# Performance work log

Hardware: AMD Instinct MI355X
Metric: run time of the kernel (lower is better)

Reference implementation:

```python
import jax, jax.numpy as jnp
import numpy as np

B = 1024
N_NODES = 30
E_PER = 82
IN_F = 128
HID = 256
HEADS = (3, 2, 1)
N_EH = 41


def _lin(k, fi, fo):
    s = 1.0 / np.sqrt(fi)
    kw, kb = jax.random.split(k)
    W = jax.random.uniform(kw, (fi, fo), jnp.float32, -s, s)
    b = jax.random.uniform(kb, (fo,), jnp.float32, -s, s)
    return W, b


def setup_inputs() -> dict:
    key = jax.random.key(0)
    ks = list(jax.random.split(key, 32))
    rng = np.random.default_rng(0)
    # base 30-node graph with E_PER directed edges, no self-loops
    src = rng.integers(0, N_NODES, E_PER)
    dst = (src + rng.integers(1, N_NODES, E_PER)) % N_NODES
    base = np.stack([src, dst])  # [2, E_PER]
    offs = (np.arange(B) * N_NODES)[None, None, :]  # [1,1,B]
    ei = (base[:, :, None] + offs).transpose(0, 2, 1).reshape(2, -1)  # [2, B*E_PER]
    e_h = rng.choice(E_PER, N_EH, replace=False)
    d = {}
    d["x"] = jax.random.normal(ks[0], (B * N_NODES, IN_F), jnp.float32)
    d["edge_index"] = jnp.asarray(ei, dtype=jnp.int32)
    d["e_h_pairs"] = jnp.asarray(base[:, e_h].T, dtype=jnp.int32)  # [N_EH, 2]
    d["Wp"], d["bp"] = _lin(ks[1], IN_F, HID)
    i = 2
    for l, H in enumerate(HEADS):
        d[f"ln_g{l}"] = jnp.ones((HID,), jnp.float32)
        d[f"ln_b{l}"] = jnp.zeros((HID,), jnp.float32)
        d[f"Wl{l}"], d[f"bl{l}"] = _lin(ks[i], HID, H * HID); i += 1
        d[f"Wr{l}"], d[f"br{l}"] = _lin(ks[i], HID, H * HID); i += 1
        d[f"att{l}"] = jax.random.normal(ks[i], (H, HID), jnp.float32) * 0.1; i += 1
        d[f"bias{l}"] = jnp.zeros((HID,), jnp.float32)
    dims = [2 * HID, 256, 128, 128, 1]
    for j in range(4):
        d[f"Wm{j}"], d[f"bm{j}"] = _lin(ks[i], dims[j], dims[j + 1]); i += 1
    return d


def _layer_norm(h, g, b):
    mu = jnp.mean(h, -1, keepdims=True)
    var = jnp.mean((h - mu) ** 2, -1, keepdims=True)
    return (h - mu) * jax.lax.rsqrt(var + 1e-5) * g + b


def _gatv2(h, src, dst, n, Wl, bl, Wr, br, att, bias):
    # PyG GATv2Conv, concat=False (mean over heads), self-loops already in src/dst
    H, C = att.shape
    xl = (h @ Wl + bl).reshape(-1, H, C)  # source transform
    xr = (h @ Wr + br).reshape(-1, H, C)  # target transform
    xj = xl[src]                          # [E,H,C]
    e = jax.nn.leaky_relu(xj + xr[dst], 0.2)
    logits = jnp.einsum('ehc,hc->eh', e, att)  # [E,H]
    m = jax.lax.stop_gradient(jax.ops.segment_max(logits, dst, num_segments=n))
    ex = jnp.exp(logits - m[dst])
    denom = jax.ops.segment_sum(ex, dst, num_segments=n)
    alpha = ex / denom[dst]               # softmax over incoming edges of dst
    out = jax.ops.segment_sum(xj * alpha[..., None], dst, num_segments=n)  # [N,H,C]
    return jnp.mean(out, 1) + bias


def reference(x, edge_index, e_h_pairs, Wp, bp,
              ln_g0, ln_b0, Wl0, bl0, Wr0, br0, att0, bias0,
              ln_g1, ln_b1, Wl1, bl1, Wr1, br1, att1, bias1,
              ln_g2, ln_b2, Wl2, bl2, Wr2, br2, att2, bias2,
              Wm0, bm0, Wm1, bm1, Wm2, bm2, Wm3, bm3):
    n = x.shape[0]
    loops = jnp.arange(n, dtype=edge_index.dtype)
    src = jnp.concatenate([edge_index[0], loops])
    dst = jnp.concatenate([edge_index[1], loops])
    lrelu = lambda v: jax.nn.leaky_relu(v, 0.01)
    h = x @ Wp + bp
    layers = [(ln_g0, ln_b0, Wl0, bl0, Wr0, br0, att0, bias0),
              (ln_g1, ln_b1, Wl1, bl1, Wr1, br1, att1, bias1),
              (ln_g2, ln_b2, Wl2, bl2, Wr2, br2, att2, bias2)]
    for (g, b, Wl, bl, Wr, br, att, bias) in layers:
        hn = _layer_norm(h, g, b)
        hc = _gatv2(hn, src, dst, n, Wl, bl, Wr, br, att, bias)
        h = lrelu(hc) + h  # dropout is identity in eval
    hb = h.reshape(-1, N_NODES, HID)  # [B, 30, 256]
    ef = jnp.concatenate([hb[:, e_h_pairs[:, 0], :], hb[:, e_h_pairs[:, 1], :]], -1)
    o = ef.reshape(-1, 2 * HID)
    o = lrelu(o @ Wm0 + bm0)
    o = lrelu(o @ Wm1 + bm1)
    o = lrelu(o @ Wm2 + bm2)
    o = o @ Wm3 + bm3
    return o.reshape(-1)
```

## Files before the change

### kernel.cpp

```cpp
#include <hip/hip_runtime.h>
#include <hip/hip_bf16.h>
#include <math.h>

#define N_NODES 30
#define E_BASE  82
#define E_TOT   112
#define B_GRAPH 1024
#define HID     256
#define NTOT    (B_GRAPH * N_NODES)
#define MAXIN   32
#define N_EH    41
#define M_MLP   (B_GRAPH * N_EH)

#define META_SRC  0
#define META_DST  E_TOT
#define META_CNT  (2 * E_TOT)
#define META_LIST 256
#define META_INTS 1216

typedef __attribute__((ext_vector_type(8))) short bf16x8;
typedef __attribute__((ext_vector_type(4))) short bf16x4;
typedef __attribute__((ext_vector_type(4))) float f32x4;
#define AS3 __attribute__((address_space(3)))
#define AS1 __attribute__((address_space(1)))

__device__ __forceinline__ void gload_lds16(const void* g, void* l) {
  __builtin_amdgcn_global_load_lds((const AS1 void*)g, (AS3 void*)l, 16, 0, 0);
}

__device__ __forceinline__ float b2f(short s) {
  union { unsigned u; float f; } x;
  x.u = ((unsigned)(unsigned short)s) << 16;
  return x.f;
}

__global__ void build_graph(const int* __restrict__ ei, int* __restrict__ meta) {
  __shared__ int cnt[N_NODES];
  int tid = threadIdx.x;
  if (tid < N_NODES) cnt[tid] = 0;
  __syncthreads();
  if (tid < E_TOT) {
    int s, d;
    if (tid < E_BASE) { s = ei[tid]; d = ei[B_GRAPH * E_BASE + tid]; }
    else              { s = tid - E_BASE; d = s; }
    meta[META_SRC + tid] = s;
    meta[META_DST + tid] = d;
    int pos = atomicAdd(&cnt[d], 1);
    if (pos < MAXIN) meta[META_LIST + d * MAXIN + pos] = tid;
  }
  __syncthreads();
  if (tid < N_NODES) meta[META_CNT + tid] = cnt[tid];
}

struct WtJob { const float* in; int K, N, tstart, ooff; };
struct WtArgs { WtJob j[10]; };

__global__ __launch_bounds__(256)
void transpose_weights(WtArgs args, __hip_bfloat16* __restrict__ out) {
  int b = blockIdx.x;
  int ji = 0;
  #pragma unroll
  for (int i = 1; i < 10; i++) if (b >= args.j[i].tstart) ji = i;
  WtJob jb = args.j[ji];
  int t = b - jb.tstart;
  int ntn = jb.N >> 5;
  int tk = t / ntn, tn = t - tk * ntn;
  int k0 = tk * 32, n0 = tn * 32;
  __shared__ float s[32][33];
  int tx = threadIdx.x & 31, ty = threadIdx.x >> 5;
  #pragma unroll
  for (int p = 0; p < 4; p++)
    s[ty + p * 8][tx] = jb.in[(size_t)(k0 + ty + p * 8) * jb.N + n0 + tx];
  __syncthreads();
  __hip_bfloat16* o = out + jb.ooff;
  #pragma unroll
  for (int p = 0; p < 4; p++) {
    int n = ty + p * 8;
    o[(size_t)(n0 + n) * jb.K + k0 + tx] = __float2bfloat16(s[tx][n]);
  }
}

template<int ACT, int OUTBF>
__device__ __forceinline__ void store4(void* Cv, size_t row, int colbase, int N,
                                       const f32x4 a, const float* bias,
                                       const float* bias2, int N1) {
  const float* bp = (colbase < N1) ? bias + colbase : bias2 + (colbase - N1);
  float4 bv = *(const float4*)bp;
  float v0 = a[0] + bv.x, v1 = a[1] + bv.y, v2 = a[2] + bv.z, v3 = a[3] + bv.w;
  if (ACT) {
    v0 = v0 > 0.f ? v0 : 0.01f * v0; v1 = v1 > 0.f ? v1 : 0.01f * v1;
    v2 = v2 > 0.f ? v2 : 0.01f * v2; v3 = v3 > 0.f ? v3 : 0.01f * v3;
  }
  if (OUTBF) {
    union { __hip_bfloat16 t[4]; uint2 u; } P;
    P.t[0] = __float2bfloat16(v0); P.t[1] = __float2bfloat16(v1);
    P.t[2] = __float2bfloat16(v2); P.t[3] = __float2bfloat16(v3);
    *(uint2*)&((__hip_bfloat16*)Cv)[row * N + colbase] = P.u;
  } else {
    float4 o = {v0, v1, v2, v3};
    *(float4*)&((float*)Cv)[row * N + colbase] = o;
  }
}

template<int ACT, int OUTBF>
__global__ __launch_bounds__(256)
void gemm_mfma(const __hip_bfloat16* __restrict__ A, const __hip_bfloat16* __restrict__ Bt,
               const float* __restrict__ bias, const float* __restrict__ bias2,
               void* __restrict__ Cv, int M, int K, int N, int N1)
{
  __shared__ __hip_bfloat16 sA[128 * 32];
  __shared__ __hip_bfloat16 sB[128 * 32];
  const int tid = threadIdx.x;
  const int lane = tid & 63;
  const int wave = tid >> 6;
  const int wx = wave & 1, wy = wave >> 1;
  const int bm = blockIdx.x, bn = blockIdx.y;
  const int mrow = lane & 15, quad = lane >> 4;

  const int r0 = tid >> 2, kc0 = (tid & 3) * 8;
  const __hip_bfloat16* Ag0 = A + (size_t)(bm * 128 + r0) * K + kc0;
  const __hip_bfloat16* Ag1 = A + (size_t)(bm * 128 + r0 + 64) * K + kc0;
  const __hip_bfloat16* Bg0 = Bt + (size_t)(bn * 128 + r0) * K + kc0;
  const __hip_bfloat16* Bg1 = Bt + (size_t)(bn * 128 + r0 + 64) * K + kc0;

  f32x4 acc[4][4];
  #pragma unroll
  for (int i = 0; i < 4; i++)
    #pragma unroll
    for (int j = 0; j < 4; j++)
      acc[i][j] = (f32x4){0.f, 0.f, 0.f, 0.f};

  for (int kt = 0; kt < K; kt += 32) {
    __syncthreads();
    gload_lds16(Ag0 + kt, &sA[tid * 8]);
    gload_lds16(Ag1 + kt, &sA[2048 + tid * 8]);
    gload_lds16(Bg0 + kt, &sB[tid * 8]);
    gload_lds16(Bg1 + kt, &sB[2048 + tid * 8]);
    __syncthreads();

    bf16x8 af[4], bfr[4];
    #pragma unroll
    for (int i = 0; i < 4; i++) {
      af[i]  = *(const bf16x8*)&sA[(wy * 64 + i * 16 + mrow) * 32 + quad * 8];
      bfr[i] = *(const bf16x8*)&sB[(wx * 64 + i * 16 + mrow) * 32 + quad * 8];
    }
    #pragma unroll
    for (int i = 0; i < 4; i++)
      #pragma unroll
      for (int j = 0; j < 4; j++)
        acc[i][j] = __builtin_amdgcn_mfma_f32_16x16x32_bf16(bfr[j], af[i], acc[i][j], 0, 0, 0);
  }

  #pragma unroll
  for (int i = 0; i < 4; i++) {
    size_t row = (size_t)bm * 128 + wy * 64 + i * 16 + mrow;
    #pragma unroll
    for (int j = 0; j < 4; j++) {
      int colbase = bn * 128 + wx * 64 + j * 16 + quad * 4;
      store4<ACT, OUTBF>(Cv, row, colbase, N, acc[i][j], bias, bias2, N1);
    }
  }
}

template<int ACT, int OUTBF>
__global__ __launch_bounds__(256)
void gemm_mfma_f32a(const float* __restrict__ A, const __hip_bfloat16* __restrict__ Bt,
                    const float* __restrict__ bias, void* __restrict__ Cv,
                    int M, int K, int N)
{
  __shared__ __hip_bfloat16 sA[128 * 32];
  __shared__ __hip_bfloat16 sB[128 * 32];
  const int tid = threadIdx.x;
  const int lane = tid & 63;
  const int wave = tid >> 6;
  const int wx = wave & 1, wy = wave >> 1;
  const int bm = blockIdx.x, bn = blockIdx.y;
  const int mrow = lane & 15, quad = lane >> 4;

  const int r0 = tid >> 2, kc0 = (tid & 3) * 8;
  const float* Ag0 = A + (size_t)(bm * 128 + r0) * K + kc0;
  const float* Ag1 = A + (size_t)(bm * 128 + r0 + 64) * K + kc0;
  const __hip_bfloat16* Bg0 = Bt + (size_t)(bn * 128 + r0) * K + kc0;
  const __hip_bfloat16* Bg1 = Bt + (size_t)(bn * 128 + r0 + 64) * K + kc0;

  f32x4 acc[4][4];
  #pragma unroll
  for (int i = 0; i < 4; i++)
    #pragma unroll
    for (int j = 0; j < 4; j++)
      acc[i][j] = (f32x4){0.f, 0.f, 0.f, 0.f};

  for (int kt = 0; kt < K; kt += 32) {
    float4 a00 = *(const float4*)(Ag0 + kt);
    float4 a01 = *(const float4*)(Ag0 + kt + 4);
    float4 a10 = *(const float4*)(Ag1 + kt);
    float4 a11 = *(const float4*)(Ag1 + kt + 4);
    __syncthreads();
    {
      __hip_bfloat16 t[8];
      t[0] = __float2bfloat16(a00.x); t[1] = __float2bfloat16(a00.y);
      t[2] = __float2bfloat16(a00.z); t[3] = __float2bfloat16(a00.w);
      t[4] = __float2bfloat16(a01.x); t[5] = __float2bfloat16(a01.y);
      t[6] = __float2bfloat16(a01.z); t[7] = __float2bfloat16(a01.w);
      *(bf16x8*)&sA[tid * 8] = *(bf16x8*)t;
      t[0] = __float2bfloat16(a10.x); t[1] = __float2bfloat16(a10.y);
      t[2] = __float2bfloat16(a10.z); t[3] = __float2bfloat16(a10.w);
      t[4] = __float2bfloat16(a11.x); t[5] = __float2bfloat16(a11.y);
      t[6] = __float2bfloat16(a11.z); t[7] = __float2bfloat16(a11.w);
      *(bf16x8*)&sA[2048 + tid * 8] = *(bf16x8*)t;
    }
    gload_lds16(Bg0 + kt, &sB[tid * 8]);
    gload_lds16(Bg1 + kt, &sB[2048 + tid * 8]);
    __syncthreads();

    bf16x8 af[4], bfr[4];
    #pragma unroll
    for (int i = 0; i < 4; i++) {
      af[i]  = *(const bf16x8*)&sA[(wy * 64 + i * 16 + mrow) * 32 + quad * 8];
      bfr[i] = *(const bf16x8*)&sB[(wx * 64 + i * 16 + mrow) * 32 + quad * 8];
    }
    #pragma unroll
    for (int i = 0; i < 4; i++)
      #pragma unroll
      for (int j = 0; j < 4; j++)
        acc[i][j] = __builtin_amdgcn_mfma_f32_16x16x32_bf16(bfr[j], af[i], acc[i][j], 0, 0, 0);
  }

  #pragma unroll
  for (int i = 0; i < 4; i++) {
    size_t row = (size_t)bm * 128 + wy * 64 + i * 16 + mrow;
    #pragma unroll
    for (int j = 0; j < 4; j++) {
      int colbase = bn * 128 + wx * 64 + j * 16 + quad * 4;
      store4<ACT, OUTBF>(Cv, row, colbase, N, acc[i][j], bias, bias, N);
    }
  }
}

__global__ __launch_bounds__(256)
void gemm_mfma_pair(const float* __restrict__ h, const int* __restrict__ pairs,
                    const __hip_bfloat16* __restrict__ Bt, const float* __restrict__ bias,
                    __hip_bfloat16* __restrict__ C, int N)
{
  const int K = 512;
  __shared__ __hip_bfloat16 sA[128 * 32];
  __shared__ __hip_bfloat16 sB[128 * 32];
  const int tid = threadIdx.x;
  const int lane = tid & 63;
  const int wave = tid >> 6;
  const int wx = wave & 1, wy = wave >> 1;
  const int bm = blockIdx.x, bn = blockIdx.y;
  const int mrow = lane & 15, quad = lane >> 4;

  const float* pu[2]; const float* pv[2]; int sub[2];
  #pragma unroll
  for (int cI = 0; cI < 2; cI++) {
    int c = tid + cI * 256;
    int r0 = c >> 2; sub[cI] = (c & 3) * 8;
    int R = bm * 128 + r0;
    int b = R / N_EH, p = R - b * N_EH;
    int u = pairs[p * 2], v = pairs[p * 2 + 1];
    pu[cI] = h + ((size_t)b * N_NODES + u) * HID;
    pv[cI] = h + ((size_t)b * N_NODES + v) * HID;
  }

  const int r0 = tid >> 2, kc0 = (tid & 3) * 8;
  const __hip_bfloat16* Bg0 = Bt + (size_t)(bn * 128 + r0) * K + kc0;
  const __hip_bfloat16* Bg1 = Bt + (size_t)(bn * 128 + r0 + 64) * K + kc0;

  f32x4 acc[4][4];
  #pragma unroll
  for (int i = 0; i < 4; i++)
    #pragma unroll
    for (int j = 0; j < 4; j++)
      acc[i][j] = (f32x4){0.f, 0.f, 0.f, 0.f};

  for (int kt = 0; kt < K; kt += 32) {
    float4 av[2][2];
    #pragma unroll
    for (int cI = 0; cI < 2; cI++) {
      const float* src = (kt < 256 ? pu[cI] + kt : pv[cI] + kt - 256) + sub[cI];
      av[cI][0] = *(const float4*)src;
      av[cI][1] = *(const float4*)(src + 4);
    }
    __syncthreads();
    #pragma unroll
    for (int cI = 0; cI < 2; cI++) {
      __hip_bfloat16 t[8];
      t[0] = __float2bfloat16(av[cI][0].x); t[1] = __float2bfloat16(av[cI][0].y);
      t[2] = __float2bfloat16(av[cI][0].z); t[3] = __float2bfloat16(av[cI][0].w);
      t[4] = __float2bfloat16(av[cI][1].x); t[5] = __float2bfloat16(av[cI][1].y);
      t[6] = __float2bfloat16(av[cI][1].z); t[7] = __float2bfloat16(av[cI][1].w);
      *(bf16x8*)&sA[(tid + cI * 256) * 8] = *(bf16x8*)t;
    }
    gload_lds16(Bg0 + kt, &sB[tid * 8]);
    gload_lds16(Bg1 + kt, &sB[2048 + tid * 8]);
    __syncthreads();

    bf16x8 af[4], bfr[4];
    #pragma unroll
    for (int i = 0; i < 4; i++) {
      af[i]  = *(const bf16x8*)&sA[(wy * 64 + i * 16 + mrow) * 32 + quad * 8];
      bfr[i] = *(const bf16x8*)&sB[(wx * 64 + i * 16 + mrow) * 32 + quad * 8];
    }
    #pragma unroll
    for (int i = 0; i < 4; i++)
      #pragma unroll
      for (int j = 0; j < 4; j++)
        acc[i][j] = __builtin_amdgcn_mfma_f32_16x16x32_bf16(bfr[j], af[i], acc[i][j], 0, 0, 0);
  }

  #pragma unroll
  for (int i = 0; i < 4; i++) {
    size_t row = (size_t)bm * 128 + wy * 64 + i * 16 + mrow;
    #pragma unroll
    for (int j = 0; j < 4; j++) {
      int colbase = bn * 128 + wx * 64 + j * 16 + quad * 4;
      store4<1, 1>(C, row, colbase, N, acc[i][j], bias, bias, N);
    }
  }
}

__global__ __launch_bounds__(256)
void layernorm(const float* __restrict__ h, const float* __restrict__ g,
               const float* __restrict__ b, __hip_bfloat16* __restrict__ hn)
{
  const int wv = threadIdx.x >> 6, lane = threadIdx.x & 63;
  const size_t row = (size_t)blockIdx.x * 4 + wv;
  const float* hr = h + row * HID;
  float v[4];
  float sum = 0.f;
  #pragma unroll
  for (int j = 0; j < 4; j++) { v[j] = hr[lane + 64 * j]; sum += v[j]; }
  #pragma unroll
  for (int off = 32; off; off >>= 1) sum += __shfl_xor(sum, off);
  float mu = sum * (1.f / 256.f);
  float vs = 0.f;
  #pragma unroll
  for (int j = 0; j < 4; j++) { float d = v[j] - mu; vs += d * d; }
  #pragma unroll
  for (int off = 32; off; off >>= 1) vs += __shfl_xor(vs, off);
  float rs = rsqrtf(vs * (1.f / 256.f) + 1e-5f);
  __hip_bfloat16* outr = hn + row * HID;
  #pragma unroll
  for (int j = 0; j < 4; j++) {
    int c = lane + 64 * j;
    outr[c] = __float2bfloat16((v[j] - mu) * rs * g[c] + b[c]);
  }
}

__global__ __launch_bounds__(256)
void gat_alpha(const __hip_bfloat16* __restrict__ xcat,
               const float* __restrict__ att, float* __restrict__ alphaG,
               const int* __restrict__ meta, int H)
{
  __shared__ float slog[E_TOT];
  __shared__ float smax[N_NODES];
  __shared__ float sden[N_NODES];
  __shared__ int ssrc[E_TOT], sdst[E_TOT], scnt[N_NODES], slist[N_NODES * MAXIN];

  const int tid = threadIdx.x;
  const int g = blockIdx.x, hh = blockIdx.y;
  const size_t nodebase = (size_t)g * N_NODES;
  const int S = 2 * H * HID;

  if (tid < E_TOT) { ssrc[tid] = meta[META_SRC + tid]; sdst[tid] = meta[META_DST + tid]; }
  if (tid < N_NODES) { scnt[tid] = meta[META_CNT + tid]; sden[tid] = 0.f; }
  for (int i = tid; i < N_NODES * MAXIN; i += 256) slist[i] = meta[META_LIST + i];

  const int wv = tid >> 6, l32 = tid & 31, esub = (tid >> 5) & 1;
  const int c0 = l32 * 8;
  float attr[8];
  #pragma unroll
  for (int j = 0; j < 8; j++) attr[j] = att[hh * HID + c0 + j];
  __syncthreads();

  #pragma unroll
  for (int pass = 0; pass < 14; pass++) {
    int e = pass * 8 + wv * 2 + esub;
    int s = ssrc[e], d = sdst[e];
    bf16x8 a = *(const bf16x8*)&xcat[(nodebase + s) * S + hh * HID + c0];
    bf16x8 b = *(const bf16x8*)&xcat[(nodebase + d) * S + (H + hh) * HID + c0];
    float sum = 0.f;
    #pragma unroll
    for (int j = 0; j < 8; j++) {
      float v = b2f(a[j]) + b2f(b[j]);
      v = v > 0.f ? v : 0.2f * v;
      sum += v * attr[j];
    }
    #pragma unroll
    for (int off = 16; off; off >>= 1) sum += __shfl_xor(sum, off);
    if (l32 == 0) slog[e] = sum;
  }
  __syncthreads();

  if (tid < N_NODES) {
    int cnt = scnt[tid];
    const int* lst = &slist[tid * MAXIN];
    float m = -1e30f;
    for (int i = 0; i < cnt; i++) m = fmaxf(m, slog[lst[i]]);
    smax[tid] = m;
  }
  __syncthreads();
  if (tid < E_TOT) {
    float ex = expf(slog[tid] - smax[sdst[tid]]);
    slog[tid] = ex;
    atomicAdd(&sden[sdst[tid]], ex);
  }
  __syncthreads();
  if (tid < E_TOT)
    alphaG[((size_t)g * H + hh) * E_TOT + tid] = slog[tid] / sden[sdst[tid]];
}

template<int DO_LN>
__global__ __launch_bounds__(256, 4)
void gat_agg(const __hip_bfloat16* __restrict__ xcat, const float* __restrict__ alphaG,
             const float* __restrict__ bias, float* __restrict__ h,
             const float* __restrict__ lnG, const float* __restrict__ lnB,
             __hip_bfloat16* __restrict__ hn, const int* __restrict__ meta, int H)
{
  __shared__ __hip_bfloat16 sxl[2][N_NODES * HID];
  __shared__ float salpha[2][E_TOT];
  __shared__ int ssrc[E_TOT], scnt[N_NODES], slist[N_NODES * MAXIN];

  const int tid = threadIdx.x;
  const int g = blockIdx.x;
  const size_t nodebase = (size_t)g * N_NODES;
  const int S = 2 * H * HID;
  const int c4 = tid & 63;
  const int ng = tid >> 6;

  if (tid < E_TOT) ssrc[tid] = meta[META_SRC + tid];
  if (tid < N_NODES) scnt[tid] = meta[META_CNT + tid];
  for (int i = tid; i < N_NODES * MAXIN; i += 256) slist[i] = meta[META_LIST + i];

  float4 hres[8];
  #pragma unroll
  for (int ki = 0; ki < 8; ki++) {
    int k = ng + ki * 4;
    if (k < N_NODES) hres[ki] = *(const float4*)&h[(nodebase + k) * HID + c4 * 4];
  }

  {
    int i = tid;
    #pragma unroll
    for (int p = 0; p < 4; p++, i += 256) {
      if (i < N_NODES * HID / 8) {
        int node = i >> 5, c = (i & 31) * 8;
        gload_lds16(&xcat[(nodebase + node) * S + 0 * HID + c], &sxl[0][(size_t)i * 8]);
      }
    }
    if (tid < E_TOT) salpha[0][tid] = alphaG[((size_t)g * H + 0) * E_TOT + tid];
  }

  float acc[8][4];
  #pragma unroll
  for (int ki = 0; ki < 8; ki++)
    #pragma unroll
    for (int j = 0; j < 4; j++) acc[ki][j] = 0.f;

  for (int hh = 0; hh < H; hh++) {
    const int buf = hh & 1;
    __syncthreads();
    if (hh + 1 < H) {
      const int nb = buf ^ 1;
      int i = tid;
      #pragma unroll
      for (int p = 0; p < 4; p++, i += 256) {
        if (i < N_NODES * HID / 8) {
          int node = i >> 5, c = (i & 31) * 8;
          gload_lds16(&xcat[(nodebase + node) * S + (hh + 1) * HID + c], &sxl[nb][(size_t)i * 8]);
        }
      }
      if (tid < E_TOT) salpha[nb][tid] = alphaG[((size_t)g * H + hh + 1) * E_TOT + tid];
    }
    #pragma unroll
    for (int ki = 0; ki < 8; ki++) {
      int k = ng + ki * 4;
      if (k < N_NODES) {
        int cnt = scnt[k];
        const int* lst = &slist[k * MAXIN];
        for (int i = 0; i < cnt; i++) {
          int e = lst[i];
          float al = salpha[buf][e];
          bf16x4 v = *(const bf16x4*)&sxl[buf][ssrc[e] * HID + c4 * 4];
          acc[ki][0] += al * b2f(v[0]);
          acc[ki][1] += al * b2f(v[1]);
          acc[ki][2] += al * b2f(v[2]);
          acc[ki][3] += al * b2f(v[3]);
        }
      }
    }
  }

  const float invH = 1.f / (float)H;
  const float4 bs = *(const float4*)&bias[c4 * 4];
  float4 gv, bv;
  if (DO_LN) {
    gv = *(const float4*)&lnG[c4 * 4];
    bv = *(const float4*)&lnB[c4 * 4];
  }
  #pragma unroll
  for (int ki = 0; ki < 8; ki++) {
    int k = ng + ki * 4;
    if (k < N_NODES) {
      float o0 = acc[ki][0] * invH + bs.x; o0 = o0 > 0.f ? o0 : 0.01f * o0; o0 += hres[ki].x;
      float o1 = acc[ki][1] * invH + bs.y; o1 = o1 > 0.f ? o1 : 0.01f * o1; o1 += hres[ki].y;
      float o2 = acc[ki][2] * invH + bs.z; o2 = o2 > 0.f ? o2 : 0.01f * o2; o2 += hres[ki].z;
      float o3 = acc[ki][3] * invH + bs.w; o3 = o3 > 0.f ? o3 : 0.01f * o3; o3 += hres[ki].w;
      float4 o4 = {o0, o1, o2, o3};
      *(float4*)&h[(nodebase + k) * HID + c4 * 4] = o4;
      if (DO_LN) {
        float sum = o0 + o1 + o2 + o3;
        #pragma unroll
        for (int off = 32; off; off >>= 1) sum += __shfl_xor(sum, off);
        float mu = sum * (1.f / 256.f);
        float d0 = o0 - mu, d1 = o1 - mu, d2 = o2 - mu, d3 = o3 - mu;
        float vs = d0 * d0 + d1 * d1 + d2 * d2 + d3 * d3;
        #pragma unroll
        for (int off = 32; off; off >>= 1) vs += __shfl_xor(vs, off);
        float rs = rsqrtf(vs * (1.f / 256.f) + 1e-5f);
        __hip_bfloat16 t[4];
        t[0] = __float2bfloat16(d0 * rs * gv.x + bv.x);
        t[1] = __float2bfloat16(d1 * rs * gv.y + bv.y);
        t[2] = __float2bfloat16(d2 * rs * gv.z + bv.z);
        t[3] = __float2bfloat16(d3 * rs * gv.w + bv.w);
        *(bf16x4*)&hn[(nodebase + k) * HID + c4 * 4] = *(bf16x4*)t;
      }
    }
  }
}

__global__ __launch_bounds__(256)
void mlp_out(const float* __restrict__ o3, const float* __restrict__ w,
             const float* __restrict__ b3, float* __restrict__ out)
{
  const int wv = threadIdx.x >> 6, lane = threadIdx.x & 63;
  const int row = blockIdx.x * 4 + wv;
  const float* orow = o3 + (size_t)row * 128;
  float s = orow[lane] * w[lane] + orow[lane + 64] * w[lane + 64];
  #pragma unroll
  for (int off = 32; off; off >>= 1) s += __shfl_xor(s, off);
  if (lane == 0) out[row] = s + b3[0];
}

extern "C" void kernel_launch(void* const* d_in, const int* in_sizes, int n_in,
                              void* d_out, int out_size, void* d_ws, size_t ws_size,
                              hipStream_t stream) {
  const float* x     = (const float*)d_in[0];
  const int*   ei    = (const int*)d_in[1];
  const int*   pairs = (const int*)d_in[2];
  const float* bp    = (const float*)d_in[4];
  const float *lng[3], *lnb[3], *bl[3], *br[3], *att[3], *bias[3];
  const float *WlF[3], *WrF[3];
  for (int l = 0; l < 3; l++) {
    int base = 5 + l * 8;
    lng[l]  = (const float*)d_in[base + 0];
    lnb[l]  = (const float*)d_in[base + 1];
    WlF[l]  = (const float*)d_in[base + 2];
    bl[l]   = (const float*)d_in[base + 3];
    WrF[l]  = (const float*)d_in[base + 4];
    br[l]   = (const float*)d_in[base + 5];
    att[l]  = (const float*)d_in[base + 6];
    bias[l] = (const float*)d_in[base + 7];
  }
  const float* WmF[4] = {(const float*)d_in[29], (const float*)d_in[31],
                         (const float*)d_in[33], (const float*)d_in[35]};
  const float* bm[4] = {(const float*)d_in[30], (const float*)d_in[32],
                        (const float*)d_in[34], (const float*)d_in[36]};

  float* ws  = (float*)d_ws;
  float* h   = ws;
  __hip_bfloat16* hnb = (__hip_bfloat16*)(ws + 7864320);
  __hip_bfloat16* xcat = (__hip_bfloat16*)(ws + 11796480);
  float* alphaG = ws + 35389440;
  __hip_bfloat16* wbuf = (__hip_bfloat16*)(ws + 35733504);
  int*   meta = (int*)(ws + 36233216);
  __hip_bfloat16* o1b = (__hip_bfloat16*)xcat;
  __hip_bfloat16* o2b = (__hip_bfloat16*)(ws + 17170432);
  float* o3 = ws + 23592960;
  float* out = (float*)d_out;

  const int oWp = 0, oWl0 = 32768, oWr0 = 229376, oWl1 = 425984, oWr1 = 557056;
  const int oWl2 = 688128, oWr2 = 753664, oWm0 = 819200, oWm1 = 950272, oWm2 = 983040;

  build_graph<<<1, 128, 0, stream>>>(ei, meta);

  WtArgs wa;
  wa.j[0] = {(const float*)d_in[3], 128, 256,   0, oWp };
  wa.j[1] = {WlF[0],              256, 768,  32, oWl0};
  wa.j[2] = {WrF[0],              256, 768, 224, oWr0};
  wa.j[3] = {WlF[1],              256, 512, 416, oWl1};
  wa.j[4] = {WrF[1],              256, 512, 544, oWr1};
  wa.j[5] = {WlF[2],              256, 256, 672, oWl2};
  wa.j[6] = {WrF[2],              256, 256, 736, oWr2};
  wa.j[7] = {WmF[0],              512, 256, 800, oWm0};
  wa.j[8] = {WmF[1],              256, 128, 928, oWm1};
  wa.j[9] = {WmF[2],              128, 128, 960, oWm2};
  transpose_weights<<<976, 256, 0, stream>>>(wa, wbuf);

  gemm_mfma_f32a<0, 0><<<dim3(NTOT / 128, 2), 256, 0, stream>>>(x, wbuf + oWp, bp, h,
                                                                NTOT, 128, 256);

  layernorm<<<NTOT / 4, 256, 0, stream>>>(h, lng[0], lnb[0], hnb);

  const int Hs[3] = {3, 2, 1};
  const int oWl[3] = {oWl0, oWl1, oWl2};
  for (int l = 0; l < 3; l++) {
    int N = 2 * Hs[l] * HID;
    gemm_mfma<0, 1><<<dim3(NTOT / 128, N / 128), 256, 0, stream>>>(
        hnb, wbuf + oWl[l], bl[l], br[l], xcat, NTOT, HID, N, N / 2);
    gat_alpha<<<dim3(B_GRAPH, Hs[l]), 256, 0, stream>>>(xcat, att[l], alphaG, meta, Hs[l]);
    if (l < 2)
      gat_agg<1><<<B_GRAPH, 256, 0, stream>>>(xcat, alphaG, bias[l], h,
                                              lng[l + 1], lnb[l + 1], hnb, meta, Hs[l]);
    else
      gat_agg<0><<<B_GRAPH, 256, 0, stream>>>(xcat, alphaG, bias[l], h,
                                              nullptr, nullptr, nullptr, meta, Hs[l]);
  }

  gemm_mfma_pair<<<dim3(M_MLP / 128, 2), 256, 0, stream>>>(h, pairs, wbuf + oWm0, bm[0], o1b, 256);
  gemm_mfma<1, 1><<<dim3(M_MLP / 128, 1), 256, 0, stream>>>(o1b, wbuf + oWm1, bm[1], bm[1], o2b,
                                                            M_MLP, 256, 128, 128);
  gemm_mfma<1, 0><<<dim3(M_MLP / 128, 1), 256, 0, stream>>>(o2b, wbuf + oWm2, bm[2], bm[2], o3,
                                                            M_MLP, 128, 128, 128);
  mlp_out<<<M_MLP / 4, 256, 0, stream>>>(o3, WmF[3], bm[3], out);
}
```

Before: 500.2 us.

## Stage per-graph node features in LDS for attention and transpose MFMA epilogue

In gat_alpha, each block now bulk-loads the 30 source and target feature rows for its head into shared memory with async global-to-LDS copies, then reads edge gathers from LDS instead of global memory. The GEMM kernels swap the MFMA operand order, so each lane now holds a column of the output tile, and the epilogue is rewritten to store scalar elements per row instead of 4-wide vectors. The LDS staging adds about 30KB of shared memory per block, which may lower occupancy. The scalar epilogue stores are narrower and less coalesced than the previous vector stores.

```diff
diff --git a/kernel.cpp b/kernel.cpp
--- a/kernel.cpp
+++ b/kernel.cpp
@@ -77,28 +77,6 @@
   for (int p = 0; p < 4; p++) {
     int n = ty + p * 8;
     o[(size_t)(n0 + n) * jb.K + k0 + tx] = __float2bfloat16(s[tx][n]);
-  }
-}
-
-template<int ACT, int OUTBF>
-__device__ __forceinline__ void store4(void* Cv, size_t row, int colbase, int N,
-                                       const f32x4 a, const float* bias,
-                                       const float* bias2, int N1) {
-  const float* bp = (colbase < N1) ? bias + colbase : bias2 + (colbase - N1);
-  float4 bv = *(const float4*)bp;
-  float v0 = a[0] + bv.x, v1 = a[1] + bv.y, v2 = a[2] + bv.z, v3 = a[3] + bv.w;
-  if (ACT) {
-    v0 = v0 > 0.f ? v0 : 0.01f * v0; v1 = v1 > 0.f ? v1 : 0.01f * v1;
-    v2 = v2 > 0.f ? v2 : 0.01f * v2; v3 = v3 > 0.f ? v3 : 0.01f * v3;
-  }
-  if (OUTBF) {
-    union { __hip_bfloat16 t[4]; uint2 u; } P;
-    P.t[0] = __float2bfloat16(v0); P.t[1] = __float2bfloat16(v1);
-    P.t[2] = __float2bfloat16(v2); P.t[3] = __float2bfloat16(v3);
-    *(uint2*)&((__hip_bfloat16*)Cv)[row * N + colbase] = P.u;
-  } else {
-    float4 o = {v0, v1, v2, v3};
-    *(float4*)&((float*)Cv)[row * N + colbase] = o;
   }
 }
 
@@ -148,16 +126,23 @@
     for (int i = 0; i < 4; i++)
       #pragma unroll
       for (int j = 0; j < 4; j++)
-        acc[i][j] = __builtin_amdgcn_mfma_f32_16x16x32_bf16(bfr[j], af[i], acc[i][j], 0, 0, 0);
+        acc[i][j] = __builtin_amdgcn_mfma_f32_16x16x32_bf16(af[i], bfr[j], acc[i][j], 0, 0, 0);
   }
 
   #pragma unroll
   for (int i = 0; i < 4; i++) {
-    size_t row = (size_t)bm * 128 + wy * 64 + i * 16 + mrow;
-    #pragma unroll
-    for (int j = 0; j < 4; j++) {
-      int colbase = bn * 128 + wx * 64 + j * 16 + quad * 4;
-      store4<ACT, OUTBF>(Cv, row, colbase, N, acc[i][j], bias, bias2, N1);
+    #pragma unroll
+    for (int r = 0; r < 4; r++) {
+      size_t row = (size_t)bm * 128 + wy * 64 + i * 16 + quad * 4 + r;
+      #pragma unroll
+      for (int j = 0; j < 4; j++) {
+        int col = bn * 128 + wx * 64 + j * 16 + mrow;
+        float bc = (col < N1) ? bias[col] : bias2[col - N1];
+        float v = acc[i][j][r] + bc;
+        if (ACT) v = v > 0.f ? v : 0.01f * v;
+        if (OUTBF) ((__hip_bfloat16*)Cv)[row * N + col] = __float2bfloat16(v);
+        else       ((float*)Cv)[row * N + col] = v;
+      }
     }
   }
 }
@@ -223,16 +208,22 @@
     for (int i = 0; i < 4; i++)
       #pragma unroll
       for (int j = 0; j < 4; j++)
-        acc[i][j] = __builtin_amdgcn_mfma_f32_16x16x32_bf16(bfr[j], af[i], acc[i][j], 0, 0, 0);
+        acc[i][j] = __builtin_amdgcn_mfma_f32_16x16x32_bf16(af[i], bfr[j], acc[i][j], 0, 0, 0);
   }
 
   #pragma unroll
   for (int i = 0; i < 4; i++) {
-    size_t row = (size_t)bm * 128 + wy * 64 + i * 16 + mrow;
-    #pragma unroll
-    for (int j = 0; j < 4; j++) {
-      int colbase = bn * 128 + wx * 64 + j * 16 + quad * 4;
-      store4<ACT, OUTBF>(Cv, row, colbase, N, acc[i][j], bias, bias, N);
+    #pragma unroll
+    for (int r = 0; r < 4; r++) {
+      size_t row = (size_t)bm * 128 + wy * 64 + i * 16 + quad * 4 + r;
+      #pragma unroll
+      for (int j = 0; j < 4; j++) {
+        int col = bn * 128 + wx * 64 + j * 16 + mrow;
+        float v = acc[i][j][r] + bias[col];
+        if (ACT) v = v > 0.f ? v : 0.01f * v;
+        if (OUTBF) ((__hip_bfloat16*)Cv)[row * N + col] = __float2bfloat16(v);
+        else       ((float*)Cv)[row * N + col] = v;
+      }
     }
   }
 }
@@ -307,16 +298,21 @@
     for (int i = 0; i < 4; i++)
       #pragma unroll
       for (int j = 0; j < 4; j++)
-        acc[i][j] = __builtin_amdgcn_mfma_f32_16x16x32_bf16(bfr[j], af[i], acc[i][j], 0, 0, 0);
+        acc[i][j] = __builtin_amdgcn_mfma_f32_16x16x32_bf16(af[i], bfr[j], acc[i][j], 0, 0, 0);
   }
 
   #pragma unroll
   for (int i = 0; i < 4; i++) {
-    size_t row = (size_t)bm * 128 + wy * 64 + i * 16 + mrow;
-    #pragma unroll
-    for (int j = 0; j < 4; j++) {
-      int colbase = bn * 128 + wx * 64 + j * 16 + quad * 4;
-      store4<1, 1>(C, row, colbase, N, acc[i][j], bias, bias, N);
+    #pragma unroll
+    for (int r = 0; r < 4; r++) {
+      size_t row = (size_t)bm * 128 + wy * 64 + i * 16 + quad * 4 + r;
+      #pragma unroll
+      for (int j = 0; j < 4; j++) {
+        int col = bn * 128 + wx * 64 + j * 16 + mrow;
+        float v = acc[i][j][r] + bias[col];
+        v = v > 0.f ? v : 0.01f * v;
+        C[row * N + col] = __float2bfloat16(v);
+      }
     }
   }
 }
@@ -354,6 +350,8 @@
                const float* __restrict__ att, float* __restrict__ alphaG,
                const int* __restrict__ meta, int H)
 {
+  __shared__ __hip_bfloat16 sxl[N_NODES * HID];
+  __shared__ __hip_bfloat16 sxr[N_NODES * HID];
   __shared__ float slog[E_TOT];
   __shared__ float smax[N_NODES];
   __shared__ float sden[N_NODES];
@@ -364,6 +362,19 @@
   const size_t nodebase = (size_t)g * N_NODES;
   const int S = 2 * H * HID;
 
+  {
+    int i = tid;
+    #pragma unroll
+    for (int p = 0; p < 4; p++, i += 256) {
+      if (i < N_NODES * HID / 8) {
+        int node = i >> 5, c = (i & 31) * 8;
+        const __hip_bfloat16* row = &xcat[(nodebase + node) * S + c];
+        gload_lds16(row + hh * HID, &sxl[(size_t)i * 8]);
+        gload_lds16(row + (H + hh) * HID, &sxr[(size_t)i * 8]);
+      }
+    }
+  }
+
   if (tid < E_TOT) { ssrc[tid] = meta[META_SRC + tid]; sdst[tid] = meta[META_DST + tid]; }
   if (tid < N_NODES) { scnt[tid] = meta[META_CNT + tid]; sden[tid] = 0.f; }
   for (int i = tid; i < N_NODES * MAXIN; i += 256) slist[i] = meta[META_LIST + i];
@@ -378,9 +389,8 @@
   #pragma unroll
   for (int pass = 0; pass < 14; pass++) {
     int e = pass * 8 + wv * 2 + esub;
-    int s = ssrc[e], d = sdst[e];
-    bf16x8 a = *(const bf16x8*)&xcat[(nodebase + s) * S + hh * HID + c0];
-    bf16x8 b = *(const bf16x8*)&xcat[(nodebase + d) * S + (H + hh) * HID + c0];
+    bf16x8 a = *(const bf16x8*)&sxl[ssrc[e] * HID + c0];
+    bf16x8 b = *(const bf16x8*)&sxr[sdst[e] * HID + c0];
     float sum = 0.f;
     #pragma unroll
     for (int j = 0; j < 8; j++) {
```

Measured after the change: 456.4 us. 1.1x faster.
